# Performance work log

Hardware: AMD Instinct MI355X
Metric: run time of the kernel (lower is better)

The kernel has to match this reference:

```python
import jax, jax.numpy as jnp
import numpy as np

N = 32768       # flattened residues (batch*seq)
DIM = 1024      # dim == channel (required by residual add)
NRES = 21       # amino-acid types
RECYCLES = 2


def _quat_to_rot(q):
    w, x, y, z = q[..., 0], q[..., 1], q[..., 2], q[..., 3]
    return jnp.stack([
        jnp.stack([1 - 2 * (y * y + z * z), 2 * (x * y - w * z), 2 * (x * z + w * y)], -1),
        jnp.stack([2 * (x * y + w * z), 1 - 2 * (x * x + z * z), 2 * (y * z - w * x)], -1),
        jnp.stack([2 * (x * z - w * y), 2 * (y * z + w * x), 1 - 2 * (x * x + y * y)], -1),
    ], -2)


def _rand_rigid(key, shape, tscale=1.0):
    # random valid rigid transforms as 4x4 homogeneous matrices
    kq, kt = jax.random.split(key)
    q = jax.random.normal(kq, shape + (4,), jnp.float32)
    q = q / jnp.linalg.norm(q, axis=-1, keepdims=True)
    rot = _quat_to_rot(q)
    t = jax.random.normal(kt, shape + (3,), jnp.float32) * tscale
    m = jnp.zeros(shape + (4, 4), jnp.float32)
    m = m.at[..., :3, :3].set(rot).at[..., :3, 3].set(t).at[..., 3, 3].set(1.0)
    return m


def setup_inputs():
    key = jax.random.key(0)
    ks = jax.random.split(key, 12)
    s = 1.0 / np.sqrt(DIM)
    return {
        "rep0": jax.random.normal(ks[0], (N, DIM), jnp.float32),
        "rep1": jax.random.normal(ks[1], (N, DIM), jnp.float32),
        "w_in": jax.random.normal(ks[2], (DIM, DIM), jnp.float32) * s,
        "b_in": jnp.zeros((DIM,), jnp.float32),
        "w1": jax.random.normal(ks[3], (DIM, DIM), jnp.float32) * s,
        "b1": jnp.zeros((DIM,), jnp.float32),
        "w2": jax.random.normal(ks[4], (DIM, DIM), jnp.float32) * s,
        "b2": jnp.zeros((DIM,), jnp.float32),
        "w_ang": jax.random.normal(ks[5], (DIM, 14), jnp.float32) * s,
        "b_ang": jnp.zeros((14,), jnp.float32),
        "rigids": _rand_rigid(ks[6], (N,), tscale=10.0),              # backbone frames
        "default_frames": _rand_rigid(ks[7], (NRES, 8), tscale=1.5), # restype_rigid_group_default_frame
        "lit_positions": jax.random.normal(ks[8], (NRES, 14, 3), jnp.float32),
        "atom_mask": (jax.random.uniform(ks[9], (NRES, 14)) > 0.2).astype(jnp.float32),
        "aatype": jax.random.randint(ks[10], (N,), 0, NRES),
        "group_idx": jax.random.randint(ks[11], (NRES, 14), 0, 8),   # restype_atom14_to_rigid_group
    }


def reference(rep0, rep1, w_in, b_in, w1, b1, w2, b2, w_ang, b_ang,
              rigids, default_frames, lit_positions, atom_mask, aatype, group_idx):
    # InputProjection: shared ReLU+Linear applied to each representation, summed
    act = (jax.nn.relu(rep0) @ w_in + b_in) + (jax.nn.relu(rep1) @ w_in + b_in)
    # ResidueBlock with residual recycles: act += Linear(ReLU(Linear(ReLU(act))))
    for _ in range(RECYCLES):
        h = jax.nn.relu(act) @ w1 + b1
        h = jax.nn.relu(h) @ w2 + b2
        act = act + h
    # TorisonAngles: Linear(dim,14) -> (N,7,2) -> l2_normalize
    ang = (jax.nn.relu(act) @ w_ang + b_ang).reshape(N, 7, 2)
    angles = ang / jnp.sqrt(jnp.maximum(jnp.sum(ang * ang, -1, keepdims=True), 1e-12))
    # torsion_angles_to_frames: prepend identity backbone angle (sin=0, cos=1)
    sin = jnp.concatenate([jnp.zeros((N, 1), angles.dtype), angles[..., 0]], 1)  # [N,8]
    cos = jnp.concatenate([jnp.ones((N, 1), angles.dtype), angles[..., 1]], 1)
    z = jnp.zeros_like(sin); one = jnp.ones_like(sin)
    rotx = jnp.stack([
        jnp.stack([one, z, z, z], -1),
        jnp.stack([z, cos, -sin, z], -1),
        jnp.stack([z, sin, cos, z], -1),
        jnp.stack([z, z, z, one], -1),
    ], -2)                                            # [N,8,4,4] rotation about x by torsion
    frames = default_frames[aatype] @ rotx            # [N,8,4,4]
    # chi2/chi3/chi4 frames are defined relative to the previous chi frame
    f5 = frames[:, 4] @ frames[:, 5]
    f6 = f5 @ frames[:, 6]
    f7 = f6 @ frames[:, 7]
    frames_to_bb = jnp.concatenate([frames[:, :5], jnp.stack([f5, f6, f7], 1)], 1)
    frames_global = rigids[:, None] @ frames_to_bb    # [N,8,4,4]
    # frames_and_literature_positions_to_atom14_pos
    gidx = group_idx[aatype]                          # [N,14] rigid-group id per atom
    f14 = jnp.take_along_axis(frames_global,
                              jnp.broadcast_to(gidx[:, :, None, None], (N, 14, 4, 4)),
                              axis=1)                 # [N,14,4,4]
    pos = lit_positions[aatype]                       # [N,14,3]
    pred = jnp.einsum('naij,naj->nai', f14[..., :3, :3], pos) + f14[..., :3, 3]
    pred = pred * atom_mask[aatype][..., None]        # [N,14,3]
    return angles, pred, frames_global
```

## Files before the change

### kernel.cpp

```cpp
#include <hip/hip_runtime.h>
#include <stdint.h>

typedef uint16_t u16;
typedef uint32_t u32;
typedef __bf16 bf16;
typedef bf16 bf16x8 __attribute__((ext_vector_type(8)));
typedef float f32x4 __attribute__((ext_vector_type(4)));

#define N_RES 32768
#define DIM 1024

__device__ __forceinline__ float b2f(u16 u) {
  u32 v = ((u32)u) << 16;
  float f;
  __builtin_memcpy(&f, &v, 4);
  return f;
}
__device__ __forceinline__ u16 f2b(float f) {
  u32 u;
  __builtin_memcpy(&u, &f, 4);
  u += 0x7fffu + ((u >> 16) & 1u);
  return (u16)(u >> 16);
}
__device__ __forceinline__ void split2(float v, u16& h, u16& l) {
  h = f2b(v);
  l = f2b(v - b2f(h));
}
__device__ __forceinline__ void relu_mask4(uint4& h, uint4& l) {
  u32 s, m;
  s = h.x & 0x80008000u; m = ((s >> 15) & 0x00010001u) * 0xFFFFu; h.x &= ~m; l.x &= ~m;
  s = h.y & 0x80008000u; m = ((s >> 15) & 0x00010001u) * 0xFFFFu; h.y &= ~m; l.y &= ~m;
  s = h.z & 0x80008000u; m = ((s >> 15) & 0x00010001u) * 0xFFFFu; h.z &= ~m; l.z &= ~m;
  s = h.w & 0x80008000u; m = ((s >> 15) & 0x00010001u) * 0xFFFFu; h.w &= ~m; l.w &= ~m;
}
__device__ __forceinline__ void relu_split8(bf16x8& h, bf16x8& l) {
  uint4 uh, ul;
  __builtin_memcpy(&uh, &h, 16);
  __builtin_memcpy(&ul, &l, 16);
  relu_mask4(uh, ul);
  __builtin_memcpy(&h, &uh, 16);
  __builtin_memcpy(&l, &ul, 16);
}
__device__ __forceinline__ void split8(const float* v, uint4& H, uint4& L) {
  u16 h[8], l[8];
#pragma unroll
  for (int i = 0; i < 8; ++i) split2(v[i], h[i], l[i]);
  H.x = (u32)h[0] | ((u32)h[1] << 16);
  H.y = (u32)h[2] | ((u32)h[3] << 16);
  H.z = (u32)h[4] | ((u32)h[5] << 16);
  H.w = (u32)h[6] | ((u32)h[7] << 16);
  L.x = (u32)l[0] | ((u32)l[1] << 16);
  L.y = (u32)l[2] | ((u32)l[3] << 16);
  L.z = (u32)l[4] | ((u32)l[5] << 16);
  L.w = (u32)l[6] | ((u32)l[7] << 16);
}

__device__ __forceinline__ void g2l16(const void* g, void* lds) {
  __builtin_amdgcn_global_load_lds(
      (__attribute__((address_space(1))) void*)(g),
      (__attribute__((address_space(3))) void*)(lds), 16, 0, 0);
}

__global__ __launch_bounds__(256) void transpose_split(const float* __restrict__ in,
                                                       u16* __restrict__ outh,
                                                       u16* __restrict__ outl) {
  __shared__ float t[32][33];
  const int bx = blockIdx.x * 32, by = blockIdx.y * 32;
  const int tx = threadIdx.x, ty = threadIdx.y;
  for (int i = ty; i < 32; i += 8) t[i][tx] = in[(size_t)(by + i) * DIM + bx + tx];
  __syncthreads();
  for (int i = ty; i < 32; i += 8) {
    u16 h, l;
    split2(t[tx][i], h, l);
    const size_t o = (size_t)(bx + i) * DIM + by + tx;
    outh[o] = h;
    outl[o] = l;
  }
}

__global__ __launch_bounds__(256) void prep_input(const float* __restrict__ rep0,
                                                  const float* __restrict__ rep1,
                                                  u16* __restrict__ oh,
                                                  u16* __restrict__ ol) {
  const size_t base = ((size_t)blockIdx.x * 256 + threadIdx.x) * 8;
  float4 x0 = *(const float4*)(rep0 + base);
  float4 x1 = *(const float4*)(rep0 + base + 4);
  float4 y0 = *(const float4*)(rep1 + base);
  float4 y1 = *(const float4*)(rep1 + base + 4);
  float v[8];
  v[0] = fmaxf(x0.x, 0.f) + fmaxf(y0.x, 0.f);
  v[1] = fmaxf(x0.y, 0.f) + fmaxf(y0.y, 0.f);
  v[2] = fmaxf(x0.z, 0.f) + fmaxf(y0.z, 0.f);
  v[3] = fmaxf(x0.w, 0.f) + fmaxf(y0.w, 0.f);
  v[4] = fmaxf(x1.x, 0.f) + fmaxf(y1.x, 0.f);
  v[5] = fmaxf(x1.y, 0.f) + fmaxf(y1.y, 0.f);
  v[6] = fmaxf(x1.z, 0.f) + fmaxf(y1.z, 0.f);
  v[7] = fmaxf(x1.w, 0.f) + fmaxf(y1.w, 0.f);
  uint4 H, L;
  split8(v, H, L);
  *(uint4*)(oh + base) = H;
  *(uint4*)(ol + base) = L;
}

__global__ __launch_bounds__(256, 2) void gemm_split(
    const u16* __restrict__ Ah, const u16* __restrict__ Al, int reluA,
    const u16* __restrict__ Bh, const u16* __restrict__ Bl,
    const float* __restrict__ bias, float bscale,
    const u16* __restrict__ Rh, const u16* __restrict__ Rl,
    u16* __restrict__ Oh, u16* __restrict__ Ol) {
  __shared__ __align__(16) u32 SMEM[8192];
  u16* AS = (u16*)SMEM;
  u16* BS = (u16*)SMEM + 8192;
  u32* C_lds = SMEM;

  const int tid = threadIdx.x;
  const int wave = tid >> 6;
  const int lane = tid & 63;
  const int lrow = lane & 15;
  const int lquad = lane >> 4;

  const int g = blockIdx.x + (blockIdx.y << 3);
  const int xcd = g & 7;
  const int j = g >> 3;
  const int bm = (xcd * 32 + (j >> 3)) * 128;
  const int bn = (j & 7) * 128;

  const int wm = (wave & 1) * 64;
  const int wn = (wave >> 1) * 64;

  f32x4 acc[4][4];
#pragma unroll
  for (int i = 0; i < 4; ++i)
#pragma unroll
    for (int jj = 0; jj < 4; ++jj) acc[i][jj] = (f32x4){0.f, 0.f, 0.f, 0.f};

  const int srow = tid >> 3;
  const int dc = (tid & 7) ^ (srow & 7);
  const size_t scol = (size_t)(dc & 3) * 8;
  const u16* srcA = ((dc < 4) ? Ah : Al) + (size_t)(bm + srow) * DIM + scol;
  const u16* srcB = ((dc < 4) ? Bh : Bl) + (size_t)(bn + srow) * DIM + scol;
  u16* dA = AS + (size_t)tid * 8;
  u16* dB = BS + (size_t)tid * 8;

  const int swzH = ((lquad ^ (lrow & 7)) * 8);
  const int swzL = swzH ^ 32;

  for (int kt = 0; kt < 32; ++kt) {
    const size_t ko = (size_t)kt * 32;
#pragma unroll
    for (int is = 0; is < 4; ++is) {
      g2l16(srcA + ko + (size_t)is * 32 * DIM, dA + is * 2048);
      g2l16(srcB + ko + (size_t)is * 32 * DIM, dB + is * 2048);
    }
    __syncthreads();

    bf16x8 a_h[4], a_l[4], b_h[4], b_l[4];
#pragma unroll
    for (int i = 0; i < 4; ++i) {
      const u16* arow = AS + (wm + i * 16 + lrow) * 64;
      a_h[i] = *(const bf16x8*)(arow + swzH);
      a_l[i] = *(const bf16x8*)(arow + swzL);
      if (reluA) relu_split8(a_h[i], a_l[i]);
    }
#pragma unroll
    for (int jj = 0; jj < 4; ++jj) {
      const u16* brow = BS + (wn + jj * 16 + lrow) * 64;
      b_h[jj] = *(const bf16x8*)(brow + swzH);
      b_l[jj] = *(const bf16x8*)(brow + swzL);
    }
#pragma unroll
    for (int i = 0; i < 4; ++i)
#pragma unroll
      for (int jj = 0; jj < 4; ++jj) {
        acc[i][jj] = __builtin_amdgcn_mfma_f32_16x16x32_bf16(a_h[i], b_h[jj], acc[i][jj], 0, 0, 0);
        acc[i][jj] = __builtin_amdgcn_mfma_f32_16x16x32_bf16(a_h[i], b_l[jj], acc[i][jj], 0, 0, 0);
        acc[i][jj] = __builtin_amdgcn_mfma_f32_16x16x32_bf16(a_l[i], b_h[jj], acc[i][jj], 0, 0, 0);
      }
    __syncthreads();
  }

#pragma unroll
  for (int half = 0; half < 2; ++half) {
    if (wm == half * 64) {
#pragma unroll
      for (int jj = 0; jj < 4; ++jj) {
        const int colL = wn + jj * 16 + lrow;
        const float bj = bias[bn + colL] * bscale;
#pragma unroll
        for (int i = 0; i < 4; ++i) {
#pragma unroll
          for (int r = 0; r < 4; ++r) {
            const int row = i * 16 + lquad * 4 + r;
            u16 h, l;
            split2(acc[i][jj][r] + bj, h, l);
            C_lds[row * 128 + (colL ^ ((row & 7) << 2))] = (u32)h | ((u32)l << 16);
          }
        }
      }
    }
    __syncthreads();
    {
      const int r64 = tid & 63;
      const int wv = tid >> 6;
      const int grow = bm + half * 64 + r64;
      const int swz = (r64 & 7) << 2;
      const u32* crow = C_lds + r64 * 128;
      const size_t gbase = (size_t)grow * DIM + bn + wv * 32;
#pragma unroll
      for (int g2 = 0; g2 < 4; ++g2) {
        const int cb = wv * 32 + g2 * 8;
        uint4 qa = *(const uint4*)&crow[cb ^ swz];
        uint4 qb = *(const uint4*)&crow[(cb + 4) ^ swz];
        float v[8];
        v[0] = b2f((u16)(qa.x & 0xFFFF)) + b2f((u16)(qa.x >> 16));
        v[1] = b2f((u16)(qa.y & 0xFFFF)) + b2f((u16)(qa.y >> 16));
        v[2] = b2f((u16)(qa.z & 0xFFFF)) + b2f((u16)(qa.z >> 16));
        v[3] = b2f((u16)(qa.w & 0xFFFF)) + b2f((u16)(qa.w >> 16));
        v[4] = b2f((u16)(qb.x & 0xFFFF)) + b2f((u16)(qb.x >> 16));
        v[5] = b2f((u16)(qb.y & 0xFFFF)) + b2f((u16)(qb.y >> 16));
        v[6] = b2f((u16)(qb.z & 0xFFFF)) + b2f((u16)(qb.z >> 16));
        v[7] = b2f((u16)(qb.w & 0xFFFF)) + b2f((u16)(qb.w >> 16));
        if (Rh) {
          uint4 rh = *(const uint4*)(Rh + gbase + g2 * 8);
          uint4 rl = *(const uint4*)(Rl + gbase + g2 * 8);
          v[0] += b2f((u16)(rh.x & 0xFFFF)) + b2f((u16)(rl.x & 0xFFFF));
          v[1] += b2f((u16)(rh.x >> 16)) + b2f((u16)(rl.x >> 16));
          v[2] += b2f((u16)(rh.y & 0xFFFF)) + b2f((u16)(rl.y & 0xFFFF));
          v[3] += b2f((u16)(rh.y >> 16)) + b2f((u16)(rl.y >> 16));
          v[4] += b2f((u16)(rh.z & 0xFFFF)) + b2f((u16)(rl.z & 0xFFFF));
          v[5] += b2f((u16)(rh.z >> 16)) + b2f((u16)(rl.z >> 16));
          v[6] += b2f((u16)(rh.w & 0xFFFF)) + b2f((u16)(rl.w & 0xFFFF));
          v[7] += b2f((u16)(rh.w >> 16)) + b2f((u16)(rl.w >> 16));
        }
        uint4 H, L;
        split8(v, H, L);
        *(uint4*)(Oh + gbase + g2 * 8) = H;
        *(uint4*)(Ol + gbase + g2 * 8) = L;
      }
    }
    __syncthreads();
  }
}

__global__ __launch_bounds__(256) void angles_split(
    const u16* __restrict__ ACTh, const u16* __restrict__ ACTl,
    const u16* __restrict__ WAh, const u16* __restrict__ WAl,
    const float* __restrict__ b_ang, float* __restrict__ out_angles) {
  const int tid = threadIdx.x;
  const int wave = tid >> 6, lane = tid & 63;
  const int lrow = lane & 15, lquad = lane >> 4;
  const int rowA = blockIdx.x * 64 + wave * 16 + lrow;
  f32x4 acc = (f32x4){0.f, 0.f, 0.f, 0.f};
  const u16* gah = ACTh + (size_t)rowA * DIM + lquad * 8;
  const u16* gal = ACTl + (size_t)rowA * DIM + lquad * 8;
  const u16* gbh = WAh + (size_t)lrow * DIM + lquad * 8;
  const u16* gbl = WAl + (size_t)lrow * DIM + lquad * 8;
#pragma unroll 4
  for (int kb = 0; kb < DIM; kb += 32) {
    bf16x8 ah = *(const bf16x8*)(gah + kb);
    bf16x8 al = *(const bf16x8*)(gal + kb);
    relu_split8(ah, al);
    bf16x8 bh = *(const bf16x8*)(gbh + kb);
    bf16x8 bl = *(const bf16x8*)(gbl + kb);
    acc = __builtin_amdgcn_mfma_f32_16x16x32_bf16(ah, bh, acc, 0, 0, 0);
    acc = __builtin_amdgcn_mfma_f32_16x16x32_bf16(ah, bl, acc, 0, 0, 0);
    acc = __builtin_amdgcn_mfma_f32_16x16x32_bf16(al, bh, acc, 0, 0, 0);
  }
  const int col = lrow;
  const float bj = (col < 14) ? b_ang[col] : 0.f;
#pragma unroll
  for (int r = 0; r < 4; ++r) {
    float v = acc[r] + bj;
    float p = __shfl_xor(v, 1, 64);
    float s2 = fmaxf(v * v + p * p, 1e-12f);
    float o = v * rsqrtf(s2);
    const int orow = blockIdx.x * 64 + wave * 16 + lquad * 4 + r;
    if (col < 14) out_angles[(size_t)orow * 14 + col] = o;
  }
}

__global__ __launch_bounds__(256) void prep_wang(const float* __restrict__ w,
                                                 u16* __restrict__ outh,
                                                 u16* __restrict__ outl) {
  for (int idx = threadIdx.x; idx < 16 * 1024; idx += 256) {
    const int n = idx & 15;
    const int k = idx >> 4;
    const float v = (n < 14) ? w[(size_t)k * 14 + n] : 0.f;
    u16 h, l;
    split2(v, h, l);
    outh[(size_t)n * DIM + k] = h;
    outl[(size_t)n * DIM + k] = l;
  }
}

__device__ __forceinline__ void mm34(const float* A, const float* B, float* O) {
#pragma unroll
  for (int r = 0; r < 3; ++r) {
#pragma unroll
    for (int c = 0; c < 4; ++c) {
      float v = A[r * 4 + 0] * B[0 * 4 + c] + A[r * 4 + 1] * B[1 * 4 + c] +
                A[r * 4 + 2] * B[2 * 4 + c];
      if (c == 3) v += A[r * 4 + 3];
      O[r * 4 + c] = v;
    }
  }
}

__global__ __launch_bounds__(256) void frames_kernel(
    const float* __restrict__ angles, const float* __restrict__ rigids,
    const float* __restrict__ dframes, const float* __restrict__ litpos,
    const float* __restrict__ amask, const int* __restrict__ aatype,
    const int* __restrict__ gidx, float* __restrict__ out_pred,
    float* __restrict__ out_frames) {
  const int n = blockIdx.x * 256 + threadIdx.x;
  const int aa = aatype[n];

  float fr[8][12];
  const float* angp = angles + (size_t)n * 14;
#pragma unroll
  for (int g = 0; g < 8; ++g) {
    float s, c;
    if (g == 0) { s = 0.f; c = 1.f; }
    else { s = angp[(g - 1) * 2]; c = angp[(g - 1) * 2 + 1]; }
    const float* D = dframes + ((size_t)aa * 8 + g) * 16;
#pragma unroll
    for (int r = 0; r < 3; ++r) {
      float d0 = D[r * 4 + 0], d1 = D[r * 4 + 1], d2 = D[r * 4 + 2], d3 = D[r * 4 + 3];
      fr[g][r * 4 + 0] = d0;
      fr[g][r * 4 + 1] = d1 * c + d2 * s;
      fr[g][r * 4 + 2] = d2 * c - d1 * s;
      fr[g][r * 4 + 3] = d3;
    }
  }
  float tmp[12];
  mm34(fr[4], fr[5], tmp);
#pragma unroll
  for (int e = 0; e < 12; ++e) fr[5][e] = tmp[e];
  mm34(fr[5], fr[6], tmp);
#pragma unroll
  for (int e = 0; e < 12; ++e) fr[6][e] = tmp[e];
  mm34(fr[6], fr[7], tmp);
#pragma unroll
  for (int e = 0; e < 12; ++e) fr[7][e] = tmp[e];

  float R[12];
  const float* rp = rigids + (size_t)n * 16;
#pragma unroll
  for (int e = 0; e < 12; ++e) R[e] = rp[e];
#pragma unroll
  for (int g = 0; g < 8; ++g) {
    mm34(R, fr[g], tmp);
#pragma unroll
    for (int e = 0; e < 12; ++e) fr[g][e] = tmp[e];
  }

  float4* of = (float4*)(out_frames + (size_t)n * 128);
#pragma unroll
  for (int g = 0; g < 8; ++g) {
    of[g * 4 + 0] = (float4){fr[g][0], fr[g][1], fr[g][2], fr[g][3]};
    of[g * 4 + 1] = (float4){fr[g][4], fr[g][5], fr[g][6], fr[g][7]};
    of[g * 4 + 2] = (float4){fr[g][8], fr[g][9], fr[g][10], fr[g][11]};
    of[g * 4 + 3] = (float4){0.f, 0.f, 0.f, 1.f};
  }

  float P[42];
#pragma unroll
  for (int a = 0; a < 14; ++a) {
    const int g = gidx[aa * 14 + a];
    float f[12];
#pragma unroll
    for (int q = 0; q < 8; ++q) {
      if (q == 0) {
#pragma unroll
        for (int e = 0; e < 12; ++e) f[e] = fr[0][e];
      } else {
        const bool sel = (g == q);
#pragma unroll
        for (int e = 0; e < 12; ++e) f[e] = sel ? fr[q][e] : f[e];
      }
    }
    const float px = litpos[((size_t)aa * 14 + a) * 3 + 0];
    const float py = litpos[((size_t)aa * 14 + a) * 3 + 1];
    const float pz = litpos[((size_t)aa * 14 + a) * 3 + 2];
    const float mk = amask[aa * 14 + a];
    P[a * 3 + 0] = (f[0] * px + f[1] * py + f[2] * pz + f[3]) * mk;
    P[a * 3 + 1] = (f[4] * px + f[5] * py + f[6] * pz + f[7]) * mk;
    P[a * 3 + 2] = (f[8] * px + f[9] * py + f[10] * pz + f[11]) * mk;
  }
  float2* op = (float2*)(out_pred + (size_t)n * 42);
#pragma unroll
  for (int i = 0; i < 21; ++i) op[i] = (float2){P[2 * i], P[2 * i + 1]};
}

__global__ __launch_bounds__(256) void ws_diag(float* __restrict__ out, float mb) {
  const int i = blockIdx.x * 256 + threadIdx.x;
  if (i < N_RES * 14) out[i] = mb;
}

extern "C" void kernel_launch(void* const* d_in, const int* in_sizes, int n_in,
                              void* d_out, int out_size, void* d_ws, size_t ws_size,
                              hipStream_t stream) {
  const float* rep0 = (const float*)d_in[0];
  const float* rep1 = (const float*)d_in[1];
  const float* w_in = (const float*)d_in[2];
  const float* b_in = (const float*)d_in[3];
  const float* w1 = (const float*)d_in[4];
  const float* b1 = (const float*)d_in[5];
  const float* w2 = (const float*)d_in[6];
  const float* b2 = (const float*)d_in[7];
  const float* w_ang = (const float*)d_in[8];
  const float* b_ang = (const float*)d_in[9];
  const float* rigids = (const float*)d_in[10];
  const float* dframes = (const float*)d_in[11];
  const float* litpos = (const float*)d_in[12];
  const float* amask = (const float*)d_in[13];
  const int* aatype = (const int*)d_in[14];
  const int* gidx = (const int*)d_in[15];

  const size_t SLOT = (size_t)N_RES * DIM;
  const size_t NEED_U16 = 4 * SLOT + 6 * (size_t)DIM * DIM + 2 * 16 * DIM;

  float* out_ang = (float*)d_out;
  float* out_pred = out_ang + (size_t)N_RES * 14;
  float* out_frames = out_pred + (size_t)N_RES * 42;

  if (ws_size < NEED_U16 * 2) {
    ws_diag<<<(N_RES * 14 + 255) / 256, 256, 0, stream>>>(
        out_ang, (float)(ws_size >> 20));
    return;
  }

  u16* ACTh = (u16*)d_ws;
  u16* ACTl = ACTh + SLOT;
  u16* Hh = ACTl + SLOT;
  u16* Hl = Hh + SLOT;
  u16* W0h = Hl + SLOT;
  u16* W0l = W0h + (size_t)DIM * DIM;
  u16* W1h = W0l + (size_t)DIM * DIM;
  u16* W1l = W1h + (size_t)DIM * DIM;
  u16* W2h = W1l + (size_t)DIM * DIM;
  u16* W2l = W2h + (size_t)DIM * DIM;
  u16* WAh = W2l + (size_t)DIM * DIM;
  u16* WAl = WAh + (size_t)16 * DIM;

  transpose_split<<<dim3(32, 32), dim3(32, 8), 0, stream>>>(w_in, W0h, W0l);
  transpose_split<<<dim3(32, 32), dim3(32, 8), 0, stream>>>(w1, W1h, W1l);
  transpose_split<<<dim3(32, 32), dim3(32, 8), 0, stream>>>(w2, W2h, W2l);
  prep_wang<<<1, 256, 0, stream>>>(w_ang, WAh, WAl);

  prep_input<<<(N_RES * DIM / 8) / 256, 256, 0, stream>>>(rep0, rep1, Hh, Hl);

  dim3 gg(DIM / 128, N_RES / 128);
  gemm_split<<<gg, 256, 0, stream>>>(Hh, Hl, 0, W0h, W0l, b_in, 2.f,
                                     nullptr, nullptr, ACTh, ACTl);
  gemm_split<<<gg, 256, 0, stream>>>(ACTh, ACTl, 1, W1h, W1l, b1, 1.f,
                                     nullptr, nullptr, Hh, Hl);
  gemm_split<<<gg, 256, 0, stream>>>(Hh, Hl, 1, W2h, W2l, b2, 1.f,
                                     ACTh, ACTl, ACTh, ACTl);
  gemm_split<<<gg, 256, 0, stream>>>(ACTh, ACTl, 1, W1h, W1l, b1, 1.f,
                                     nullptr, nullptr, Hh, Hl);
  gemm_split<<<gg, 256, 0, stream>>>(Hh, Hl, 1, W2h, W2l, b2, 1.f,
                                     ACTh, ACTl, ACTh, ACTl);

  angles_split<<<N_RES / 64, 256, 0, stream>>>(ACTh, ACTl, WAh, WAl, b_ang,
                                               out_ang);
  frames_kernel<<<N_RES / 256, 256, 0, stream>>>(out_ang, rigids, dframes, litpos,
                                                 amask, aatype, gidx, out_pred,
                                                 out_frames);
}
```

Measured before the change: 1.599 ms.

## Double-buffer A tile in LDS and load B fragments directly from global

The GEMM main loop now double-buffers the A tile in shared memory, prefetching the next k-slice while computing the current one, with manual vmcnt waits and raw barriers replacing __syncthreads. B operand fragments are read straight from global memory into registers instead of being staged through LDS, which frees LDS for the second A buffer. This aims to hide global load latency, but B reads become uncached strided loads per wave, each sitting on the critical path right before the MFMAs, and B data is no longer shared across waves through LDS.

```diff
diff --git a/kernel.cpp b/kernel.cpp
--- a/kernel.cpp
+++ b/kernel.cpp
@@ -110,7 +110,6 @@
     u16* __restrict__ Oh, u16* __restrict__ Ol) {
   __shared__ __align__(16) u32 SMEM[8192];
   u16* AS = (u16*)SMEM;
-  u16* BS = (u16*)SMEM + 8192;
   u32* C_lds = SMEM;
 
   const int tid = threadIdx.x;
@@ -138,35 +137,49 @@
   const int dc = (tid & 7) ^ (srow & 7);
   const size_t scol = (size_t)(dc & 3) * 8;
   const u16* srcA = ((dc < 4) ? Ah : Al) + (size_t)(bm + srow) * DIM + scol;
-  const u16* srcB = ((dc < 4) ? Bh : Bl) + (size_t)(bn + srow) * DIM + scol;
-  u16* dA = AS + (size_t)tid * 8;
-  u16* dB = BS + (size_t)tid * 8;
 
   const int swzH = ((lquad ^ (lrow & 7)) * 8);
   const int swzL = swzH ^ 32;
 
+  const size_t bfrag0 = (size_t)(bn + wn + lrow) * DIM + lquad * 8;
+
+  {
+    u16* dst = AS + (size_t)tid * 8;
+#pragma unroll
+    for (int is = 0; is < 4; ++is)
+      g2l16(srcA + (size_t)is * 32 * DIM, dst + is * 2048);
+  }
+
+  int p = 0;
   for (int kt = 0; kt < 32; ++kt) {
-    const size_t ko = (size_t)kt * 32;
-#pragma unroll
-    for (int is = 0; is < 4; ++is) {
-      g2l16(srcA + ko + (size_t)is * 32 * DIM, dA + is * 2048);
-      g2l16(srcB + ko + (size_t)is * 32 * DIM, dB + is * 2048);
-    }
-    __syncthreads();
-
-    bf16x8 a_h[4], a_l[4], b_h[4], b_l[4];
+    const size_t kb = (size_t)kt * 32;
+    bf16x8 b_h[4], b_l[4];
+#pragma unroll
+    for (int jj = 0; jj < 4; ++jj) {
+      const size_t bo = bfrag0 + (size_t)jj * 16 * DIM + kb;
+      b_h[jj] = *(const bf16x8*)(Bh + bo);
+      b_l[jj] = *(const bf16x8*)(Bl + bo);
+    }
+    {
+      const size_t ko = (size_t)((kt < 31) ? kt + 1 : 31) * 32;
+      u16* dst = AS + (size_t)(p ^ 1) * 8192 + (size_t)tid * 8;
+#pragma unroll
+      for (int is = 0; is < 4; ++is)
+        g2l16(srcA + ko + (size_t)is * 32 * DIM, dst + is * 2048);
+    }
+    __builtin_amdgcn_sched_barrier(0);
+    asm volatile("s_waitcnt vmcnt(12)" ::: "memory");
+    __builtin_amdgcn_s_barrier();
+    __builtin_amdgcn_sched_barrier(0);
+
+    const u16* Abuf = AS + (size_t)p * 8192;
+    bf16x8 a_h[4], a_l[4];
 #pragma unroll
     for (int i = 0; i < 4; ++i) {
-      const u16* arow = AS + (wm + i * 16 + lrow) * 64;
+      const u16* arow = Abuf + (wm + i * 16 + lrow) * 64;
       a_h[i] = *(const bf16x8*)(arow + swzH);
       a_l[i] = *(const bf16x8*)(arow + swzL);
       if (reluA) relu_split8(a_h[i], a_l[i]);
-    }
-#pragma unroll
-    for (int jj = 0; jj < 4; ++jj) {
-      const u16* brow = BS + (wn + jj * 16 + lrow) * 64;
-      b_h[jj] = *(const bf16x8*)(brow + swzH);
-      b_l[jj] = *(const bf16x8*)(brow + swzL);
     }
 #pragma unroll
     for (int i = 0; i < 4; ++i)
@@ -176,8 +189,15 @@
         acc[i][jj] = __builtin_amdgcn_mfma_f32_16x16x32_bf16(a_h[i], b_l[jj], acc[i][jj], 0, 0, 0);
         acc[i][jj] = __builtin_amdgcn_mfma_f32_16x16x32_bf16(a_l[i], b_h[jj], acc[i][jj], 0, 0, 0);
       }
-    __syncthreads();
-  }
+    __builtin_amdgcn_sched_barrier(0);
+    asm volatile("s_waitcnt lgkmcnt(0)" ::: "memory");
+    __builtin_amdgcn_s_barrier();
+    __builtin_amdgcn_sched_barrier(0);
+    p ^= 1;
+  }
+  asm volatile("s_waitcnt vmcnt(0)" ::: "memory");
+  __builtin_amdgcn_s_barrier();
+  __builtin_amdgcn_sched_barrier(0);
 
 #pragma unroll
   for (int half = 0; half < 2; ++half) {
```

New measurement: 2.018 ms. +26.2%, slower.

## Double-buffer GEMM LDS tiles and move ReLU into GEMM epilogues

Applied to the files above, without the earlier changes.

The split-bf16 GEMM now keeps two LDS stages (64KB) and prefetches the next K tile with async global-to-LDS loads while the current tile feeds the MFMAs. Explicit vmcnt waits and raw barriers replace the previous sync-per-iteration scheme. ReLU is moved from the operand load path into the epilogue of the producing GEMM (reluOut), so the consumer GEMM and the angles kernel no longer apply relu_split8 per tile. The larger LDS footprint may lower occupancy, and the hand-placed waitcnt must stay in step with the number of loads issued.

```diff
diff --git a/kernel.cpp b/kernel.cpp
--- a/kernel.cpp
+++ b/kernel.cpp
@@ -105,12 +105,11 @@
 __global__ __launch_bounds__(256, 2) void gemm_split(
     const u16* __restrict__ Ah, const u16* __restrict__ Al, int reluA,
     const u16* __restrict__ Bh, const u16* __restrict__ Bl,
-    const float* __restrict__ bias, float bscale,
+    const float* __restrict__ bias, float bscale, int reluOut,
     const u16* __restrict__ Rh, const u16* __restrict__ Rl,
     u16* __restrict__ Oh, u16* __restrict__ Ol) {
-  __shared__ __align__(16) u32 SMEM[8192];
-  u16* AS = (u16*)SMEM;
-  u16* BS = (u16*)SMEM + 8192;
+  __shared__ __align__(16) u32 SMEM[16384];
+  u16* SM = (u16*)SMEM;
   u32* C_lds = SMEM;
 
   const int tid = threadIdx.x;
@@ -139,32 +138,34 @@
   const size_t scol = (size_t)(dc & 3) * 8;
   const u16* srcA = ((dc < 4) ? Ah : Al) + (size_t)(bm + srow) * DIM + scol;
   const u16* srcB = ((dc < 4) ? Bh : Bl) + (size_t)(bn + srow) * DIM + scol;
-  u16* dA = AS + (size_t)tid * 8;
-  u16* dB = BS + (size_t)tid * 8;
 
   const int swzH = ((lquad ^ (lrow & 7)) * 8);
   const int swzL = swzH ^ 32;
 
-  for (int kt = 0; kt < 32; ++kt) {
+  auto stage = [&](int buf, int kt) {
     const size_t ko = (size_t)kt * 32;
+    u16* dA = SM + (size_t)buf * 16384 + (size_t)tid * 8;
+    u16* dB = dA + 8192;
 #pragma unroll
     for (int is = 0; is < 4; ++is) {
       g2l16(srcA + ko + (size_t)is * 32 * DIM, dA + is * 2048);
       g2l16(srcB + ko + (size_t)is * 32 * DIM, dB + is * 2048);
     }
-    __syncthreads();
-
+  };
+  auto compute = [&](int buf) {
+    const u16* rA = SM + (size_t)buf * 16384;
+    const u16* rB = rA + 8192;
     bf16x8 a_h[4], a_l[4], b_h[4], b_l[4];
 #pragma unroll
     for (int i = 0; i < 4; ++i) {
-      const u16* arow = AS + (wm + i * 16 + lrow) * 64;
+      const u16* arow = rA + (wm + i * 16 + lrow) * 64;
       a_h[i] = *(const bf16x8*)(arow + swzH);
       a_l[i] = *(const bf16x8*)(arow + swzL);
       if (reluA) relu_split8(a_h[i], a_l[i]);
     }
 #pragma unroll
     for (int jj = 0; jj < 4; ++jj) {
-      const u16* brow = BS + (wn + jj * 16 + lrow) * 64;
+      const u16* brow = rB + (wn + jj * 16 + lrow) * 64;
       b_h[jj] = *(const bf16x8*)(brow + swzH);
       b_l[jj] = *(const bf16x8*)(brow + swzL);
     }
@@ -176,8 +177,22 @@
         acc[i][jj] = __builtin_amdgcn_mfma_f32_16x16x32_bf16(a_h[i], b_l[jj], acc[i][jj], 0, 0, 0);
         acc[i][jj] = __builtin_amdgcn_mfma_f32_16x16x32_bf16(a_l[i], b_h[jj], acc[i][jj], 0, 0, 0);
       }
-    __syncthreads();
-  }
+  };
+
+  stage(0, 0);
+  for (int kt = 0; kt < 32; kt += 2) {
+    stage(1, kt + 1);
+    asm volatile("s_waitcnt vmcnt(8)" ::: "memory");
+    asm volatile("s_barrier" ::: "memory");
+    compute(0);
+    asm volatile("s_barrier" ::: "memory");
+    stage(0, (kt + 2 < 32) ? kt + 2 : 31);
+    asm volatile("s_waitcnt vmcnt(8)" ::: "memory");
+    asm volatile("s_barrier" ::: "memory");
+    compute(1);
+    asm volatile("s_barrier" ::: "memory");
+  }
+  __syncthreads();
 
 #pragma unroll
   for (int half = 0; half < 2; ++half) {
@@ -232,6 +247,10 @@
           v[6] += b2f((u16)(rh.w & 0xFFFF)) + b2f((u16)(rl.w & 0xFFFF));
           v[7] += b2f((u16)(rh.w >> 16)) + b2f((u16)(rl.w >> 16));
         }
+        if (reluOut) {
+#pragma unroll
+          for (int e = 0; e < 8; ++e) v[e] = fmaxf(v[e], 0.f);
+        }
         uint4 H, L;
         split8(v, H, L);
         *(uint4*)(Oh + gbase + g2 * 8) = H;
@@ -259,7 +278,6 @@
   for (int kb = 0; kb < DIM; kb += 32) {
     bf16x8 ah = *(const bf16x8*)(gah + kb);
     bf16x8 al = *(const bf16x8*)(gal + kb);
-    relu_split8(ah, al);
     bf16x8 bh = *(const bf16x8*)(gbh + kb);
     bf16x8 bl = *(const bf16x8*)(gbl + kb);
     acc = __builtin_amdgcn_mfma_f32_16x16x32_bf16(ah, bh, acc, 0, 0, 0);
@@ -451,15 +469,15 @@
   prep_input<<<(N_RES * DIM / 8) / 256, 256, 0, stream>>>(rep0, rep1, Hh, Hl);
 
   dim3 gg(DIM / 128, N_RES / 128);
-  gemm_split<<<gg, 256, 0, stream>>>(Hh, Hl, 0, W0h, W0l, b_in, 2.f,
+  gemm_split<<<gg, 256, 0, stream>>>(Hh, Hl, 0, W0h, W0l, b_in, 2.f, 0,
                                      nullptr, nullptr, ACTh, ACTl);
-  gemm_split<<<gg, 256, 0, stream>>>(ACTh, ACTl, 1, W1h, W1l, b1, 1.f,
+  gemm_split<<<gg, 256, 0, stream>>>(ACTh, ACTl, 1, W1h, W1l, b1, 1.f, 1,
                                      nullptr, nullptr, Hh, Hl);
-  gemm_split<<<gg, 256, 0, stream>>>(Hh, Hl, 1, W2h, W2l, b2, 1.f,
+  gemm_split<<<gg, 256, 0, stream>>>(Hh, Hl, 0, W2h, W2l, b2, 1.f, 0,
                                      ACTh, ACTl, ACTh, ACTl);
-  gemm_split<<<gg, 256, 0, stream>>>(ACTh, ACTl, 1, W1h, W1l, b1, 1.f,
+  gemm_split<<<gg, 256, 0, stream>>>(ACTh, ACTl, 1, W1h, W1l, b1, 1.f, 1,
                                      nullptr, nullptr, Hh, Hl);
-  gemm_split<<<gg, 256, 0, stream>>>(Hh, Hl, 1, W2h, W2l, b2, 1.f,
+  gemm_split<<<gg, 256, 0, stream>>>(Hh, Hl, 0, W2h, W2l, b2, 1.f, 1,
                                      ACTh, ACTl, ACTh, ACTl);
 
   angles_split<<<N_RES / 64, 256, 0, stream>>>(ACTh, ACTl, WAh, WAl, b_ang,
```

Measured after the change: 1.570 ms. About the same (-1.8%).
